# Kernel tuning notes

Hardware: AMD Instinct MI355X
Metric: run time of the kernel (lower is better)

The kernel has to match this reference:

```python
import jax, jax.numpy as jnp
import numpy as np

N = 100000   # nodes
E = 800000   # edges
D = 128      # hidden_dim (= in_dim here)
H = 4        # heads
C = D // H   # per-head channels = 32
L = 3        # gat layers


def setup_inputs() -> dict:
    key = jax.random.key(0)
    ks = jax.random.split(key, 14)
    s = 0.05
    return {
        "x": jax.random.normal(ks[0], (N, D), dtype=jnp.float32),
        "edge_index": jax.random.randint(ks[1], (2, E), 0, N, dtype=jnp.int32),
        "w_in": jax.random.normal(ks[2], (D, D), dtype=jnp.float32) * s,
        "b_in": jnp.zeros((D,), jnp.float32),
        "Wl": jax.random.normal(ks[3], (L, D, D), dtype=jnp.float32) * s,   # lin_l weights
        "bl": jnp.zeros((L, D), jnp.float32),                               # lin_l bias
        "Wr": jax.random.normal(ks[4], (L, D, D), dtype=jnp.float32) * s,   # lin_r (no bias)
        "att": jax.random.normal(ks[5], (L, H, C), dtype=jnp.float32) * s,  # attention vector a
        "b_out": jnp.zeros((L, D), jnp.float32),                            # conv output bias
        "Wres": jax.random.normal(ks[6], (L - 1, D, D), dtype=jnp.float32) * s,  # residual projs i>0
        "bres": jnp.zeros((L - 1, D), jnp.float32),
        "ln_g": jnp.ones((L, D), jnp.float32),
        "ln_b": jnp.zeros((L, D), jnp.float32),
    }


def _layer_norm(x, g, b, eps=1e-5):
    mu = x.mean(-1, keepdims=True)
    var = ((x - mu) ** 2).mean(-1, keepdims=True)
    return (x - mu) * jax.lax.rsqrt(var + eps) * g + b


def _pairnorm(x, scale=1.0):
    xc = x - x.mean(0, keepdims=True)
    l2 = jnp.sqrt((xc * xc).sum(1, keepdims=True)) + 1e-6
    return xc / l2 * scale * jnp.sqrt(jnp.float32(x.shape[0]))


def _gatv2(x, src, dst, Wl, bl, Wr, att, b_out):
    # lin_l / lin_r projections -> [N, H, C]
    xl = (x @ Wl + bl).reshape(N, H, C)
    xr = (x @ Wr).reshape(N, H, C)
    # edge-wise message: leaky_relu(x_l[j] + x_r[i])  [E, H, C]
    m = jax.nn.leaky_relu(xl[src] + xr[dst], negative_slope=0.2)
    logits = (m * att).sum(-1)  # [E, H]
    # segment softmax over edges grouped by destination node
    lmax = jax.ops.segment_max(logits, dst, num_segments=N)  # [N, H]
    a = jnp.exp(logits - lmax[dst])
    denom = jax.ops.segment_sum(a, dst, num_segments=N)
    a = a / (denom[dst] + 1e-16)
    # aggregate alpha * x_l[j] into destinations, concat heads
    out = jax.ops.segment_sum(a[:, :, None] * xl[src], dst, num_segments=N)
    return out.reshape(N, D) + b_out


def reference(x, edge_index, w_in, b_in, Wl, bl, Wr, att, b_out, Wres, bres, ln_g, ln_b):
    src, dst = edge_index[0], edge_index[1]
    h = x @ w_in + b_in
    for i in range(L):
        identity = h if i == 0 else h @ Wres[i - 1] + bres[i - 1]
        h = _gatv2(h, src, dst, Wl[i], bl[i], Wr[i], att[i], b_out[i])
        h = _pairnorm(h)
        # dropout is identity in eval mode
        h = h + identity
        h = _layer_norm(h, ln_g[i], ln_b[i])
        if i < L - 1:
            h = jax.nn.relu(h)
    return h
```

## Files before the change

### kernel.cpp

```cpp
#include <hip/hip_runtime.h>
#include <hip/hip_bf16.h>

#define NN 100000
#define NE 800000

typedef __attribute__((ext_vector_type(8))) short bf16x8;
typedef __attribute__((ext_vector_type(4))) float f32x4;
typedef unsigned short ushort_t;

static __device__ __forceinline__ short f2bf(float f) {
    union { float f; unsigned u; } v; v.f = f;
    unsigned u = v.u;
    unsigned r = u + 0x7FFFu + ((u >> 16) & 1u);
    return (short)(r >> 16);
}
static __device__ __forceinline__ float bf2f(unsigned short u) {
    union { unsigned u; float f; } v; v.u = ((unsigned)u) << 16;
    return v.f;
}

__global__ void prep_w_k(const float* __restrict__ w_in, const float* __restrict__ Wl,
                         const float* __restrict__ Wr, const float* __restrict__ Wres,
                         ushort_t* __restrict__ wt)
{
    __shared__ float tile[32][33];
    int m = blockIdx.z;
    const float* src;
    if (m == 0)      src = w_in;
    else if (m < 4)  src = Wl + (size_t)(m - 1) * 16384;
    else if (m < 7)  src = Wr + (size_t)(m - 4) * 16384;
    else             src = Wres + (size_t)(m - 7) * 16384;
    ushort_t* dst = wt + (size_t)m * 16384;

    int tx = threadIdx.x, ty = threadIdx.y;
    int k0 = blockIdx.x * 32, c0 = blockIdx.y * 32;
    #pragma unroll
    for (int j = 0; j < 4; ++j)
        tile[ty + 8 * j][tx] = src[(size_t)(k0 + ty + 8 * j) * 128 + c0 + tx];
    __syncthreads();
    #pragma unroll
    for (int j = 0; j < 4; ++j)
        dst[(size_t)(c0 + ty + 8 * j) * 128 + k0 + tx] = (ushort_t)f2bf(tile[tx][ty + 8 * j]);
}

template<int A_FP32>
__global__ __launch_bounds__(256, 4)
void gemm_k(const void* __restrict__ Av, const ushort_t* __restrict__ wt,
            int w0, int w1, int w2,
            const float* __restrict__ bias0, const float* __restrict__ bias2,
            ushort_t* __restrict__ out0, int Dout0, ushort_t* __restrict__ out2, int M)
{
    __shared__ short Bs[128][136];
    const int tid = threadIdx.x;
    const int rowBlk = blockIdx.x * 128;
    const int y = blockIdx.y;
    const ushort_t* W = wt + (size_t)((y == 0) ? w0 : (y == 1) ? w1 : w2) * 16384;
    const float* bias = (y == 0) ? bias0 : ((y == 2) ? bias2 : nullptr);
    ushort_t* out = (y == 2) ? out2 : out0;
    const int Dout   = (y == 2) ? 128 : Dout0;
    const int colOff = (y == 1) ? 128 : 0;

    const int wave = tid >> 6;
    const int lane = tid & 63;
    const int quad = lane >> 4;
    const int lr   = lane & 15;

    const int row0 = rowBlk + wave * 32 + lr;
    const int row1 = row0 + 16;

    bf16x8 afr[4][2];
    #pragma unroll
    for (int ks = 0; ks < 4; ++ks) {
        int kb = ks * 32 + quad * 8;
        bf16x8 a0 = (bf16x8)0, a1 = (bf16x8)0;
        if (A_FP32) {
            const float* A = (const float*)Av;
            if (row0 < M) {
                float4 v0 = *(const float4*)(A + (size_t)row0 * 128 + kb);
                float4 v1 = *(const float4*)(A + (size_t)row0 * 128 + kb + 4);
                a0[0]=f2bf(v0.x); a0[1]=f2bf(v0.y); a0[2]=f2bf(v0.z); a0[3]=f2bf(v0.w);
                a0[4]=f2bf(v1.x); a0[5]=f2bf(v1.y); a0[6]=f2bf(v1.z); a0[7]=f2bf(v1.w);
            }
            if (row1 < M) {
                float4 v0 = *(const float4*)(A + (size_t)row1 * 128 + kb);
                float4 v1 = *(const float4*)(A + (size_t)row1 * 128 + kb + 4);
                a1[0]=f2bf(v0.x); a1[1]=f2bf(v0.y); a1[2]=f2bf(v0.z); a1[3]=f2bf(v0.w);
                a1[4]=f2bf(v1.x); a1[5]=f2bf(v1.y); a1[6]=f2bf(v1.z); a1[7]=f2bf(v1.w);
            }
        } else {
            const ushort_t* A = (const ushort_t*)Av;
            if (row0 < M) a0 = *(const bf16x8*)(A + (size_t)row0 * 128 + kb);
            if (row1 < M) a1 = *(const bf16x8*)(A + (size_t)row1 * 128 + kb);
        }
        afr[ks][0] = a0; afr[ks][1] = a1;
    }

    #pragma unroll
    for (int i = 0; i < 8; ++i) {
        int linear = tid + 256 * i;
        int r  = linear >> 4;
        int c8 = (linear & 15) << 3;
        *(bf16x8*)&Bs[r][c8] = *(const bf16x8*)(W + (size_t)r * 128 + c8);
    }
    __syncthreads();

    f32x4 acc[2][8];
    #pragma unroll
    for (int mt = 0; mt < 2; ++mt)
        #pragma unroll
        for (int nt = 0; nt < 8; ++nt) acc[mt][nt] = (f32x4)(0.0f);

    #pragma unroll
    for (int ks = 0; ks < 4; ++ks) {
        int kb = ks * 32 + quad * 8;
        #pragma unroll
        for (int nt = 0; nt < 8; ++nt) {
            bf16x8 b = *(const bf16x8*)&Bs[nt * 16 + lr][kb];
            acc[0][nt] = __builtin_amdgcn_mfma_f32_16x16x32_bf16(afr[ks][0], b, acc[0][nt], 0, 0, 0);
            acc[1][nt] = __builtin_amdgcn_mfma_f32_16x16x32_bf16(afr[ks][1], b, acc[1][nt], 0, 0, 0);
        }
    }

    __syncthreads();
    #pragma unroll
    for (int mt = 0; mt < 2; ++mt)
        #pragma unroll
        for (int nt = 0; nt < 8; ++nt) {
            int col = nt * 16 + lr;
            float b = bias ? bias[col] : 0.0f;
            #pragma unroll
            for (int r = 0; r < 4; ++r) {
                int row = wave * 32 + mt * 16 + quad * 4 + r;
                Bs[row][col] = f2bf(acc[mt][nt][r] + b);
            }
        }
    __syncthreads();
    #pragma unroll
    for (int i = 0; i < 8; ++i) {
        int linear = tid + 256 * i;
        int r  = linear >> 4;
        int c8 = (linear & 15) << 3;
        int gr = rowBlk + r;
        if (gr < M)
            *(bf16x8*)(out + (size_t)gr * Dout + colOff + c8) = *(const bf16x8*)&Bs[r][c8];
    }
}

__global__ void count_k(const int* __restrict__ dst, int* __restrict__ deg) {
    int e = blockIdx.x * 256 + threadIdx.x;
    if (e < NE) atomicAdd(&deg[dst[e]], 1);
}

__global__ void scan1_k(const int* __restrict__ deg, int* __restrict__ excl,
                        int* __restrict__ bsum) {
    __shared__ int buf[256];
    int i = blockIdx.x * 256 + threadIdx.x;
    int v = (i < NN) ? deg[i] : 0;
    buf[threadIdx.x] = v; __syncthreads();
    for (int off = 1; off < 256; off <<= 1) {
        int t = (threadIdx.x >= off) ? buf[threadIdx.x - off] : 0;
        __syncthreads();
        buf[threadIdx.x] += t;
        __syncthreads();
    }
    if (i < NN) excl[i] = buf[threadIdx.x] - v;
    if (threadIdx.x == 255) bsum[blockIdx.x] = buf[255];
}

__global__ void scan2_k(int* __restrict__ bsum, int nb, int* __restrict__ total) {
    __shared__ int buf[512];
    int v = (threadIdx.x < nb) ? bsum[threadIdx.x] : 0;
    buf[threadIdx.x] = v; __syncthreads();
    for (int off = 1; off < 512; off <<= 1) {
        int t = (threadIdx.x >= off) ? buf[threadIdx.x - off] : 0;
        __syncthreads();
        buf[threadIdx.x] += t;
        __syncthreads();
    }
    if (threadIdx.x < nb) bsum[threadIdx.x] = buf[threadIdx.x] - v;
    if (threadIdx.x == 511) *total = buf[511];
}

__global__ void scan3_k(int* __restrict__ row_ptr, const int* __restrict__ bsum,
                        int* __restrict__ cursor) {
    int i = blockIdx.x * 256 + threadIdx.x;
    if (i < NN) {
        int v = row_ptr[i] + bsum[blockIdx.x];
        row_ptr[i] = v;
        cursor[i]  = v;
    }
}

__global__ void scatter_k(const int* __restrict__ src, const int* __restrict__ dst,
                          int* __restrict__ cursor, int* __restrict__ csr_src) {
    int e = blockIdx.x * 256 + threadIdx.x;
    if (e < NE) {
        int p = atomicAdd(&cursor[dst[e]], 1);
        csr_src[p] = src[e];
    }
}

__global__ __launch_bounds__(256, 8)
void gat_aggregate_k(const ushort_t* __restrict__ xlr, const int* __restrict__ row_ptr,
                     const int* __restrict__ csr_src, const float* __restrict__ att,
                     const float* __restrict__ b_out, ushort_t* __restrict__ g)
{
    int node = blockIdx.x * 4 + (threadIdx.x >> 6);
    int lane = threadIdx.x & 63;
    int slot = lane >> 4;
    int cl   = (lane & 15) << 3;
    bf16x8 xru = *(const bf16x8*)(xlr + (size_t)node * 256 + 128 + cl);
    float xr[8], at[8];
    #pragma unroll
    for (int j = 0; j < 8; ++j) xr[j] = bf2f((ushort_t)xru[j]);
    float4 at0 = *(const float4*)(att + cl);
    float4 at1 = *(const float4*)(att + cl + 4);
    at[0] = at0.x; at[1] = at0.y; at[2] = at0.z; at[3] = at0.w;
    at[4] = at1.x; at[5] = at1.y; at[6] = at1.z; at[7] = at1.w;

    int e0 = row_ptr[node], e1 = row_ptr[node + 1];
    float acc[8] = {0.f,0.f,0.f,0.f,0.f,0.f,0.f,0.f};
    float suma = 0.f;
    for (int e = e0; e < e1; e += 8) {
        int ea = e + slot, eb = e + 4 + slot;
        bool va = ea < e1, vb = eb < e1;
        int sa = csr_src[va ? ea : e];
        int sb = csr_src[vb ? eb : e];
        bf16x8 xua = *(const bf16x8*)(xlr + (size_t)sa * 256 + cl);
        bf16x8 xub = *(const bf16x8*)(xlr + (size_t)sb * 256 + cl);
        float xa[8], xb[8];
        #pragma unroll
        for (int j = 0; j < 8; ++j) { xa[j] = bf2f((ushort_t)xua[j]); xb[j] = bf2f((ushort_t)xub[j]); }
        float pa = 0.f, pb = 0.f;
        #pragma unroll
        for (int j = 0; j < 8; ++j) {
            float ma = xa[j] + xr[j]; ma = fmaxf(ma, 0.2f * ma);
            float mb = xb[j] + xr[j]; mb = fmaxf(mb, 0.2f * mb);
            pa = fmaf(at[j], ma, pa);
            pb = fmaf(at[j], mb, pb);
        }
        pa += __shfl_xor(pa, 1); pa += __shfl_xor(pa, 2);
        pb += __shfl_xor(pb, 1); pb += __shfl_xor(pb, 2);
        float aa = va ? __expf(pa) : 0.f;
        float ab = vb ? __expf(pb) : 0.f;
        suma += aa + ab;
        #pragma unroll
        for (int j = 0; j < 8; ++j) acc[j] = fmaf(aa, xa[j], fmaf(ab, xb[j], acc[j]));
    }
    suma += __shfl_xor(suma, 16); suma += __shfl_xor(suma, 32);
    #pragma unroll
    for (int j = 0; j < 8; ++j) {
        acc[j] += __shfl_xor(acc[j], 16);
        acc[j] += __shfl_xor(acc[j], 32);
    }
    if (slot == 0) {
        float inv = 1.0f / (suma + 1e-16f);
        float4 ob0 = *(const float4*)(b_out + cl);
        float4 ob1 = *(const float4*)(b_out + cl + 4);
        float ob[8] = {ob0.x, ob0.y, ob0.z, ob0.w, ob1.x, ob1.y, ob1.z, ob1.w};
        short r[8];
        #pragma unroll
        for (int j = 0; j < 8; ++j) r[j] = f2bf(fmaf(acc[j], inv, ob[j]));
        *(bf16x8*)(g + (size_t)node * 128 + cl) = *(const bf16x8*)r;
    }
}

__global__ void colsum_k(const ushort_t* __restrict__ g, float* __restrict__ colsum) {
    __shared__ float buf[256];
    int c = threadIdx.x & 127;
    int half = threadIdx.x >> 7;
    int r0 = blockIdx.x * 256;
    int rend = min(r0 + 256, NN);
    float s = 0.f;
    for (int r = r0 + half; r < rend; r += 2)
        s += bf2f(g[(size_t)r * 128 + c]);
    buf[threadIdx.x] = s;
    __syncthreads();
    if (threadIdx.x < 128)
        atomicAdd(&colsum[c], buf[threadIdx.x] + buf[threadIdx.x + 128]);
}

__global__ __launch_bounds__(256, 4)
void finalize_k(const ushort_t* __restrict__ g, const float* __restrict__ colsum,
                const ushort_t* __restrict__ ident, const float* __restrict__ lng,
                const float* __restrict__ lnb, ushort_t* __restrict__ hout_bf,
                float* __restrict__ hout_f32, int is_final)
{
    int node = blockIdx.x * 4 + (threadIdx.x >> 6);
    int lane = threadIdx.x & 63;
    int j0 = lane * 2;
    const float invN = 1.0f / (float)NN;
    const float sqrtN = sqrtf((float)NN);

    ushort2 vu = *(const ushort2*)(g + (size_t)node * 128 + j0);
    float x0 = bf2f(vu.x) - colsum[j0] * invN;
    float x1 = bf2f(vu.y) - colsum[j0 + 1] * invN;
    float ss = x0 * x0 + x1 * x1;
    ss += __shfl_xor(ss, 1);  ss += __shfl_xor(ss, 2);  ss += __shfl_xor(ss, 4);
    ss += __shfl_xor(ss, 8);  ss += __shfl_xor(ss, 16); ss += __shfl_xor(ss, 32);
    float sc = sqrtN / (sqrtf(ss) + 1e-6f);

    ushort2 idu = *(const ushort2*)(ident + (size_t)node * 128 + j0);
    float t0 = x0 * sc + bf2f(idu.x);
    float t1 = x1 * sc + bf2f(idu.y);

    float m = t0 + t1;
    m += __shfl_xor(m, 1);  m += __shfl_xor(m, 2);  m += __shfl_xor(m, 4);
    m += __shfl_xor(m, 8);  m += __shfl_xor(m, 16); m += __shfl_xor(m, 32);
    m *= (1.0f / 128.0f);
    float d0 = t0 - m, d1 = t1 - m;
    float vv = d0 * d0 + d1 * d1;
    vv += __shfl_xor(vv, 1);  vv += __shfl_xor(vv, 2);  vv += __shfl_xor(vv, 4);
    vv += __shfl_xor(vv, 8);  vv += __shfl_xor(vv, 16); vv += __shfl_xor(vv, 32);
    vv *= (1.0f / 128.0f);
    float r = rsqrtf(vv + 1e-5f);

    float y0 = d0 * r * lng[j0]     + lnb[j0];
    float y1 = d1 * r * lng[j0 + 1] + lnb[j0 + 1];
    if (is_final) {
        float2 o; o.x = y0; o.y = y1;
        *(float2*)(hout_f32 + (size_t)node * 128 + j0) = o;
    } else {
        y0 = fmaxf(y0, 0.f); y1 = fmaxf(y1, 0.f);
        ushort2 o; o.x = (ushort_t)f2bf(y0); o.y = (ushort_t)f2bf(y1);
        *(ushort2*)(hout_bf + (size_t)node * 128 + j0) = o;
    }
}

extern "C" void kernel_launch(void* const* d_in, const int* in_sizes, int n_in,
                              void* d_out, int out_size, void* d_ws, size_t ws_size,
                              hipStream_t stream) {
    const float* x     = (const float*)d_in[0];
    const int*   ei    = (const int*)  d_in[1];
    const float* w_in  = (const float*)d_in[2];
    const float* b_in  = (const float*)d_in[3];
    const float* Wl    = (const float*)d_in[4];
    const float* bl    = (const float*)d_in[5];
    const float* Wr    = (const float*)d_in[6];
    const float* att   = (const float*)d_in[7];
    const float* b_out = (const float*)d_in[8];
    const float* Wres  = (const float*)d_in[9];
    const float* bres  = (const float*)d_in[10];
    const float* ln_g  = (const float*)d_in[11];
    const float* ln_b  = (const float*)d_in[12];

    ushort_t* h     = (ushort_t*)d_ws;
    ushort_t* xlr   = h + (size_t)NN * 128;
    ushort_t* ident = xlr + (size_t)NN * 256;
    ushort_t* g     = ident + (size_t)NN * 128;
    ushort_t* wt    = g + (size_t)NN * 128;
    int*   row_ptr = (int*)(wt + 9 * 16384);
    int*   cursor  = row_ptr + (NN + 1);
    float* colsum  = (float*)(cursor + NN);
    int*   bsum    = (int*)(colsum + 384);
    int*   csr_src = bsum + 512;

    const int* e_src = ei;
    const int* e_dst = ei + NE;

    hipMemsetAsync(cursor, 0, (size_t)(NN + 384) * 4, stream);

    prep_w_k<<<dim3(4, 4, 9), dim3(32, 8), 0, stream>>>(w_in, Wl, Wr, Wres, wt);

    const int nb = (NN + 255) / 256;
    count_k  <<<NE / 256, 256, 0, stream>>>(e_dst, cursor);
    scan1_k  <<<nb, 256, 0, stream>>>(cursor, row_ptr, bsum);
    scan2_k  <<<1, 512, 0, stream>>>(bsum, nb, row_ptr + NN);
    scan3_k  <<<nb, 256, 0, stream>>>(row_ptr, bsum, cursor);
    scatter_k<<<NE / 256, 256, 0, stream>>>(e_src, e_dst, cursor, csr_src);

    const int gx = (NN + 127) / 128;

    gemm_k<1><<<dim3(gx, 1), 256, 0, stream>>>(x, wt, 0, 0, 0,
                                               b_in, nullptr, h, 128, nullptr, NN);

    for (int i = 0; i < 3; ++i) {
        gemm_k<0><<<dim3(gx, (i > 0) ? 3 : 2), 256, 0, stream>>>(
            h, wt, 1 + i, 4 + i, 7 + (i - 1),
            bl + i * 128, (i > 0) ? (bres + (i - 1) * 128) : nullptr,
            xlr, 256, ident, NN);
        gat_aggregate_k<<<NN / 4, 256, 0, stream>>>(xlr, row_ptr, csr_src,
                                                    att + i * 128, b_out + i * 128, g);
        colsum_k<<<nb, 256, 0, stream>>>(g, colsum + i * 128);
        finalize_k<<<NN / 4, 256, 0, stream>>>(g, colsum + i * 128,
                                               (i == 0) ? h : ident,
                                               ln_g + i * 128, ln_b + i * 128,
                                               h, (float*)d_out, (i == 2) ? 1 : 0);
    }
}
```

Before: 652.0 us.

## Decompose leaky-relu attention into linear and abs terms precomputed via GEMM

Rewrites leaky_relu(s) as 0.6*s + 0.4*|s|, so the linear part of the attention logit splits into per-node terms a·xl[j] and a·xr[i]. Those terms come from an extra projection matrix (Wl·att, Wr·att) that is computed once and multiplied alongside the main GEMM with an extra MFMA tile. The edge loop then only needs the |s| dot product plus two scalar lookups. It also drops the two-edges-per-iteration unrolling to one edge per slot, which cuts per-edge ALU work but adds an extra gather from dlr6 and a small GEMM epilogue write. The linear-term projections are rounded to bf16 before use.

Measured after the change: 719.6 us. 1.1x slower.

```diff
diff --git a/kernel.cpp b/kernel.cpp
--- a/kernel.cpp
+++ b/kernel.cpp
@@ -43,14 +43,53 @@
         dst[(size_t)(c0 + ty + 8 * j) * 128 + k0 + tx] = (ushort_t)f2bf(tile[tx][ty + 8 * j]);
 }
 
+__global__ void prep_p_k(const float* __restrict__ Wl, const float* __restrict__ Wr,
+                         const float* __restrict__ att, const float* __restrict__ bl,
+                         ushort_t* __restrict__ Pmat, float* __restrict__ qvec)
+{
+    int i = blockIdx.x;
+    int k = threadIdx.x;
+    __shared__ float at6[128];
+    __shared__ float qb[128];
+    at6[k] = 0.6f * att[i * 128 + k];
+    qb[k]  = bl[i * 128 + k];
+    __syncthreads();
+    const float* wl = Wl + (size_t)i * 16384 + (size_t)k * 128;
+    const float* wr = Wr + (size_t)i * 16384 + (size_t)k * 128;
+    float pl[4] = {0.f,0.f,0.f,0.f}, pr[4] = {0.f,0.f,0.f,0.f};
+    for (int c = 0; c < 128; ++c) {
+        int h = c >> 5;
+        pl[h] = fmaf(wl[c], at6[c], pl[h]);
+        pr[h] = fmaf(wr[c], at6[c], pr[h]);
+    }
+    ushort_t* P = Pmat + (size_t)i * 2048;
+    #pragma unroll
+    for (int h = 0; h < 4; ++h) {
+        P[(size_t)h * 128 + k]       = (ushort_t)f2bf(pl[h]);
+        P[(size_t)(4 + h) * 128 + k] = (ushort_t)f2bf(pr[h]);
+    }
+    #pragma unroll
+    for (int h = 8; h < 16; ++h) P[(size_t)h * 128 + k] = 0;
+    __syncthreads();
+    if (k < 4) {
+        float s = 0.f;
+        for (int c = 0; c < 32; ++c) s += qb[k * 32 + c] * at6[k * 32 + c];
+        qvec[i * 8 + k] = s;
+        qvec[i * 8 + 4 + k] = 0.f;
+    }
+}
+
 template<int A_FP32>
 __global__ __launch_bounds__(256, 4)
 void gemm_k(const void* __restrict__ Av, const ushort_t* __restrict__ wt,
             int w0, int w1, int w2,
             const float* __restrict__ bias0, const float* __restrict__ bias2,
-            ushort_t* __restrict__ out0, int Dout0, ushort_t* __restrict__ out2, int M)
+            ushort_t* __restrict__ out0, int Dout0, ushort_t* __restrict__ out2, int M,
+            const ushort_t* __restrict__ Pmat, const float* __restrict__ qvec,
+            float* __restrict__ dlr6)
 {
     __shared__ short Bs[128][136];
+    __shared__ short Ps[16][136];
     const int tid = threadIdx.x;
     const int rowBlk = blockIdx.x * 128;
     const int y = blockIdx.y;
@@ -59,6 +98,7 @@
     ushort_t* out = (y == 2) ? out2 : out0;
     const int Dout   = (y == 2) ? 128 : Dout0;
     const int colOff = (y == 1) ? 128 : 0;
+    const bool doP = (y == 0) && (Pmat != nullptr);
 
     const int wave = tid >> 6;
     const int lane = tid & 63;
@@ -102,6 +142,11 @@
         int c8 = (linear & 15) << 3;
         *(bf16x8*)&Bs[r][c8] = *(const bf16x8*)(W + (size_t)r * 128 + c8);
     }
+    if (doP) {
+        int r  = tid >> 4;
+        int c8 = (tid & 15) << 3;
+        *(bf16x8*)&Ps[r][c8] = *(const bf16x8*)(Pmat + (size_t)r * 128 + c8);
+    }
     __syncthreads();
 
     f32x4 acc[2][8];
@@ -109,6 +154,8 @@
     for (int mt = 0; mt < 2; ++mt)
         #pragma unroll
         for (int nt = 0; nt < 8; ++nt) acc[mt][nt] = (f32x4)(0.0f);
+    f32x4 accP[2];
+    accP[0] = (f32x4)(0.0f); accP[1] = (f32x4)(0.0f);
 
     #pragma unroll
     for (int ks = 0; ks < 4; ++ks) {
@@ -119,6 +166,22 @@
             acc[0][nt] = __builtin_amdgcn_mfma_f32_16x16x32_bf16(afr[ks][0], b, acc[0][nt], 0, 0, 0);
             acc[1][nt] = __builtin_amdgcn_mfma_f32_16x16x32_bf16(afr[ks][1], b, acc[1][nt], 0, 0, 0);
         }
+        if (doP) {
+            bf16x8 pb = *(const bf16x8*)&Ps[lr][kb];
+            accP[0] = __builtin_amdgcn_mfma_f32_16x16x32_bf16(afr[ks][0], pb, accP[0], 0, 0, 0);
+            accP[1] = __builtin_amdgcn_mfma_f32_16x16x32_bf16(afr[ks][1], pb, accP[1], 0, 0, 0);
+        }
+    }
+
+    if (doP && lr < 8) {
+        float qv = qvec[lr];
+        #pragma unroll
+        for (int mt = 0; mt < 2; ++mt)
+            #pragma unroll
+            for (int r = 0; r < 4; ++r) {
+                int row = rowBlk + wave * 32 + mt * 16 + quad * 4 + r;
+                if (row < M) dlr6[(size_t)row * 8 + lr] = accP[mt][r] + qv;
+            }
     }
 
     __syncthreads();
@@ -201,51 +264,50 @@
 }
 
 __global__ __launch_bounds__(256, 8)
-void gat_aggregate_k(const ushort_t* __restrict__ xlr, const int* __restrict__ row_ptr,
-                     const int* __restrict__ csr_src, const float* __restrict__ att,
-                     const float* __restrict__ b_out, ushort_t* __restrict__ g)
+void gat_aggregate_k(const ushort_t* __restrict__ xlr, const float* __restrict__ dlr6,
+                     const int* __restrict__ row_ptr, const int* __restrict__ csr_src,
+                     const float* __restrict__ att, const float* __restrict__ b_out,
+                     ushort_t* __restrict__ g)
 {
     int node = blockIdx.x * 4 + (threadIdx.x >> 6);
     int lane = threadIdx.x & 63;
     int slot = lane >> 4;
     int cl   = (lane & 15) << 3;
+    int head = (lane & 15) >> 2;
+
     bf16x8 xru = *(const bf16x8*)(xlr + (size_t)node * 256 + 128 + cl);
-    float xr[8], at[8];
+    float xr[8], at4[8];
     #pragma unroll
     for (int j = 0; j < 8; ++j) xr[j] = bf2f((ushort_t)xru[j]);
     float4 at0 = *(const float4*)(att + cl);
     float4 at1 = *(const float4*)(att + cl + 4);
-    at[0] = at0.x; at[1] = at0.y; at[2] = at0.z; at[3] = at0.w;
-    at[4] = at1.x; at[5] = at1.y; at[6] = at1.z; at[7] = at1.w;
+    at4[0] = 0.4f*at0.x; at4[1] = 0.4f*at0.y; at4[2] = 0.4f*at0.z; at4[3] = 0.4f*at0.w;
+    at4[4] = 0.4f*at1.x; at4[5] = 0.4f*at1.y; at4[6] = 0.4f*at1.z; at4[7] = 0.4f*at1.w;
+    float drn = dlr6[(size_t)node * 8 + 4 + head];
 
     int e0 = row_ptr[node], e1 = row_ptr[node + 1];
     float acc[8] = {0.f,0.f,0.f,0.f,0.f,0.f,0.f,0.f};
     float suma = 0.f;
-    for (int e = e0; e < e1; e += 8) {
-        int ea = e + slot, eb = e + 4 + slot;
-        bool va = ea < e1, vb = eb < e1;
+    for (int e = e0; e < e1; e += 4) {
+        int ea = e + slot;
+        bool va = ea < e1;
         int sa = csr_src[va ? ea : e];
-        int sb = csr_src[vb ? eb : e];
+        float dla = dlr6[(size_t)sa * 8 + head];
         bf16x8 xua = *(const bf16x8*)(xlr + (size_t)sa * 256 + cl);
-        bf16x8 xub = *(const bf16x8*)(xlr + (size_t)sb * 256 + cl);
-        float xa[8], xb[8];
-        #pragma unroll
-        for (int j = 0; j < 8; ++j) { xa[j] = bf2f((ushort_t)xua[j]); xb[j] = bf2f((ushort_t)xub[j]); }
-        float pa = 0.f, pb = 0.f;
+        float xa[8];
+        #pragma unroll
+        for (int j = 0; j < 8; ++j) xa[j] = bf2f((ushort_t)xua[j]);
+        float pa = 0.f;
         #pragma unroll
         for (int j = 0; j < 8; ++j) {
-            float ma = xa[j] + xr[j]; ma = fmaxf(ma, 0.2f * ma);
-            float mb = xb[j] + xr[j]; mb = fmaxf(mb, 0.2f * mb);
-            pa = fmaf(at[j], ma, pa);
-            pb = fmaf(at[j], mb, pb);
+            float s = xa[j] + xr[j];
+            pa = fmaf(at4[j], fabsf(s), pa);
         }
         pa += __shfl_xor(pa, 1); pa += __shfl_xor(pa, 2);
-        pb += __shfl_xor(pb, 1); pb += __shfl_xor(pb, 2);
-        float aa = va ? __expf(pa) : 0.f;
-        float ab = vb ? __expf(pb) : 0.f;
-        suma += aa + ab;
-        #pragma unroll
-        for (int j = 0; j < 8; ++j) acc[j] = fmaf(aa, xa[j], fmaf(ab, xb[j], acc[j]));
+        float aa = va ? __expf(pa + dla + drn) : 0.f;
+        suma += aa;
+        #pragma unroll
+        for (int j = 0; j < 8; ++j) acc[j] = fmaf(aa, xa[j], acc[j]);
     }
     suma += __shfl_xor(suma, 16); suma += __shfl_xor(suma, 32);
     #pragma unroll
@@ -354,6 +416,9 @@
     float* colsum  = (float*)(cursor + NN);
     int*   bsum    = (int*)(colsum + 384);
     int*   csr_src = bsum + 512;
+    float* dlr6    = (float*)(csr_src + NE);
+    ushort_t* Pmat = (ushort_t*)(dlr6 + (size_t)NN * 8);
+    float* qvec    = (float*)(Pmat + 3 * 2048);
 
     const int* e_src = ei;
     const int* e_dst = ei + NE;
@@ -361,6 +426,7 @@
     hipMemsetAsync(cursor, 0, (size_t)(NN + 384) * 4, stream);
 
     prep_w_k<<<dim3(4, 4, 9), dim3(32, 8), 0, stream>>>(w_in, Wl, Wr, Wres, wt);
+    prep_p_k<<<3, 128, 0, stream>>>(Wl, Wr, att, bl, Pmat, qvec);
 
     const int nb = (NN + 255) / 256;
     count_k  <<<NE / 256, 256, 0, stream>>>(e_dst, cursor);
@@ -372,14 +438,16 @@
     const int gx = (NN + 127) / 128;
 
     gemm_k<1><<<dim3(gx, 1), 256, 0, stream>>>(x, wt, 0, 0, 0,
-                                               b_in, nullptr, h, 128, nullptr, NN);
+                                               b_in, nullptr, h, 128, nullptr, NN,
+                                               nullptr, nullptr, nullptr);
 
     for (int i = 0; i < 3; ++i) {
         gemm_k<0><<<dim3(gx, (i > 0) ? 3 : 2), 256, 0, stream>>>(
             h, wt, 1 + i, 4 + i, 7 + (i - 1),
             bl + i * 128, (i > 0) ? (bres + (i - 1) * 128) : nullptr,
-            xlr, 256, ident, NN);
-        gat_aggregate_k<<<NN / 4, 256, 0, stream>>>(xlr, row_ptr, csr_src,
+            xlr, 256, ident, NN,
+            Pmat + (size_t)i * 2048, qvec + i * 8, dlr6);
+        gat_aggregate_k<<<NN / 4, 256, 0, stream>>>(xlr, dlr6, row_ptr, csr_src,
                                                     att + i * 128, b_out + i * 128, g);
         colsum_k<<<nb, 256, 0, stream>>>(g, colsum + i * 128);
         finalize_k<<<NN / 4, 256, 0, stream>>>(g, colsum + i * 128,
```
